# Performance work log

Hardware: AMD Instinct MI355X
Metric: run time of the kernel (lower is better)

The kernel has to match this reference:

```python
import jax, jax.numpy as jnp
import numpy as np

B, C, N = 1, 128, 8192
K, KNN, RES, NUM, NUM_LEVELS, BASE_SCALE = 128, 32, 3, 27, 3, 0.25


def _prelu(x, a):
    return jnp.where(x >= 0, x, a.reshape(()) * x)


def _gn(x, gamma, beta, groups, eps=1e-5):
    b, ch = x.shape[0], x.shape[1]
    xr = x.reshape(b, groups, -1)
    mu = xr.mean(axis=2, keepdims=True)
    var = xr.var(axis=2, keepdims=True)
    xn = ((xr - mu) * jax.lax.rsqrt(var + eps)).reshape(x.shape)
    shp = (1, ch) + (1,) * (x.ndim - 2)
    return xn * gamma.reshape(shp) + beta.reshape(shp)


def _conv1x1(x, W, b):
    y = jnp.einsum('oc,bc...->bo...', W, x)
    return y + b.reshape((1, -1) + (1,) * (x.ndim - 2))


def _base():
    i = np.arange(NUM)
    return jnp.asarray(np.stack([i // 9 % 3 - 1, i // 3 % 3 - 1, i % 3 - 1], 1).astype(np.float32))


def _forward(fmap1, fmap2, xyz2, coords,
             out_w1, out_b1, out_g, out_bt, out_pr, out_w2, out_b2,
             vox_w1, vox_b1, vox_g, vox_bt, vox_pr, vox_w2, vox_b2,
             knn_w1, knn_b1, knn_g, knn_bt, knn_pr, knn_ow, knn_ob):
    b, c, n_p = fmap1.shape
    sg = jax.lax.stop_gradient
    # correlation + truncation (init_module)
    corr = jnp.einsum('bcn,bcm->bnm', fmap1, fmap2) / jnp.sqrt(jnp.asarray(c, fmap1.dtype))
    tcorr, tidx = jax.lax.top_k(corr, K)                       # (b, n_p, K)
    bi = jnp.arange(b)[:, None, None]
    ni = jnp.arange(n_p)[None, :, None]
    txyz2 = xyz2[bi, tidx]                                     # (b, n_p, K, 3)
    ones = jnp.ones_like(tcorr)

    feats = []
    # multi-level voxel average pooling (scatter_add into 27 cubes)
    for i in range(NUM_LEVELS):
        r = BASE_SCALE * 2 ** i
        dv = jnp.round((txyz2 - coords[:, :, None, :]) / r)
        valid = jnp.all(jnp.abs(dv) <= 1.0, axis=-1)
        iv = dv + 1.0
        cube = (iv[..., 0] * 9 + iv[..., 1] * 3 + iv[..., 2]).astype(jnp.int32)
        cube = sg(jnp.where(valid, cube, 0))
        vf = sg(valid.astype(tcorr.dtype))
        cadd = jnp.zeros((b, n_p, NUM), tcorr.dtype).at[bi, ni, cube].add(tcorr * vf)
        ccnt = jnp.clip(jnp.zeros((b, n_p, NUM), tcorr.dtype).at[bi, ni, cube].add(ones * vf), 1, n_p)
        feats.append((cadd / ccnt).transpose(0, 2, 1))         # (b, 27, n_p)

    # coarse level: scatter_max to find per-cube center candidates (all no-grad)
    r = BASE_SCALE * 2 ** 3
    R = 2.0 * r
    sxyz, scrd = sg(txyz2), sg(coords)
    dv = jnp.round((sxyz - scrd[:, :, None, :]) / R)
    validc = jnp.all(jnp.abs(dv) <= 1.5, axis=-1)
    cidx = ((dv[..., 0] + 1.0) * 9 + (dv[..., 1] + 1.0) * 3 + (dv[..., 2] + 1.0)).astype(jnp.int32) + 1
    cidx = jnp.where(validc, cidx, 0)                          # (b, n_p, K) in [0, 27]
    vals = sg(tcorr) * validc
    masked = jnp.where(cidx[..., None] == jnp.arange(NUM + 1), vals[..., None], -jnp.inf)
    center_corr = masked.max(axis=2)[:, :, 1:]                 # (b, n_p, 27)
    center_idx = masked.argmax(axis=2)[:, :, 1:]
    mask_oob = center_corr <= 0                                # covers empty bins (-inf)
    center_idx = jnp.where(mask_oob, 0, center_idx)
    center_coord = sxyz[bi, ni, center_idx]                    # (b, n_p, 27, 3)

    base = _base()
    lim = (R - r) / 2.0
    idx_scatter = jnp.full((b, n_p, K), NUM, jnp.int32)
    moves = []
    for k in range(NUM):                                       # fixed 27-voxel loop
        vkc = (scrd + base[k] * R)[:, :, None, :]
        mv = jnp.clip(center_coord[:, :, k:k + 1, :] - vkc, -lim, lim) + vkc
        moves.append(mv)
        rep = jnp.all(jnp.abs((sxyz - mv) / r) <= 0.5, axis=-1) & ~mask_oob[:, :, k:k + 1]
        idx_scatter = jnp.where(rep, k, idx_scatter)           # later k overwrites (torch order)
    voxel_xyz = jnp.concatenate(moves, axis=2)                 # (b, n_p, 27, 3), no-grad

    cadd = jnp.zeros((b, n_p, NUM + 1), tcorr.dtype).at[bi, ni, idx_scatter].add(tcorr)
    ccnt = jnp.zeros((b, n_p, NUM + 1), tcorr.dtype).at[bi, ni, idx_scatter].add(ones)
    voxel_corr = cadd[:, :, :NUM] / jnp.clip(ccnt[:, :, :NUM], 1, n_p)

    vin = jnp.concatenate([voxel_corr[:, None], voxel_xyz.transpose(0, 3, 1, 2)], axis=1)  # (b,4,n_p,27)
    h = _prelu(_gn(_conv1x1(vin, vox_w1, vox_b1), vox_g, vox_bt, 8), vox_pr)
    h = _conv1x1(h, vox_w2, vox_b2)                            # (b,1,n_p,27)
    feats.append(h[:, 0].transpose(0, 2, 1))                   # (b,27,n_p)

    vfeat = jnp.concatenate(feats, axis=1)                     # (b,108,n_p)
    vfeat = _prelu(_gn(_conv1x1(vfeat, out_w1, out_b1), out_g, out_bt, 8), out_pr)
    voxel_out = _conv1x1(vfeat, out_w2, out_b2)                # (b,64,n_p)

    # knn branch
    dist = jnp.sum((txyz2 - coords[:, :, None, :]) ** 2, axis=-1)
    _, nbr = jax.lax.top_k(-sg(dist), KNN)                     # (b,n_p,KNN)
    knn_corr = jnp.take_along_axis(tcorr, nbr, axis=2)[:, None]            # (b,1,n_p,KNN)
    knn_xyz = txyz2[bi, ni, nbr].transpose(0, 3, 1, 2) - coords.transpose(0, 2, 1)[:, :, :, None]
    kf = _prelu(_gn(_conv1x1(jnp.concatenate([knn_corr, knn_xyz], 1), knn_w1, knn_b1), knn_g, knn_bt, 8), knn_pr)
    kf = kf.max(axis=3)                                        # (b,64,n_p)
    return voxel_out + _conv1x1(kf, knn_ow, knn_ob)


def setup_inputs() -> dict:
    key = jax.random.key(0)
    ks = jax.random.split(key, 26)
    xyz2 = jax.random.uniform(ks[0], (B, N, 3), jnp.float32, -3.0, 3.0)
    coords = xyz2 + 0.3 * jax.random.normal(ks[1], (B, N, 3), jnp.float32)
    w = lambda k, s, sc=0.1: sc * jax.random.normal(k, s, jnp.float32)
    return {
        'fmap1': jax.random.normal(ks[2], (B, C, N), jnp.float32),
        'fmap2': jax.random.normal(ks[3], (B, C, N), jnp.float32),
        'xyz2': xyz2, 'coords': coords,
        'out_w1': w(ks[4], (128, 108)), 'out_b1': w(ks[5], (128,)),
        'out_g': 1.0 + w(ks[6], (128,), 0.05), 'out_bt': w(ks[7], (128,), 0.05),
        'out_pr': jnp.full((1,), 0.25, jnp.float32),
        'out_w2': w(ks[8], (64, 128)), 'out_b2': w(ks[9], (64,)),
        'vox_w1': w(ks[10], (32, 4)), 'vox_b1': w(ks[11], (32,)),
        'vox_g': 1.0 + w(ks[12], (32,), 0.05), 'vox_bt': w(ks[13], (32,), 0.05),
        'vox_pr': jnp.full((1,), 0.25, jnp.float32),
        'vox_w2': w(ks[14], (1, 32)), 'vox_b2': w(ks[15], (1,)),
        'knn_w1': w(ks[16], (64, 4)), 'knn_b1': w(ks[17], (64,)),
        'knn_g': 1.0 + w(ks[18], (64,), 0.05), 'knn_bt': w(ks[19], (64,), 0.05),
        'knn_pr': jnp.full((1,), 0.25, jnp.float32),
        'knn_ow': w(ks[20], (64, 64)), 'knn_ob': w(ks[21], (64,)),
    }


def reference(fmap1, fmap2, xyz2, coords,
              out_w1, out_b1, out_g, out_bt, out_pr, out_w2, out_b2,
              vox_w1, vox_b1, vox_g, vox_bt, vox_pr, vox_w2, vox_b2,
              knn_w1, knn_b1, knn_g, knn_bt, knn_pr, knn_ow, knn_ob):
    return _forward(fmap1, fmap2, xyz2, coords,
                    out_w1, out_b1, out_g, out_bt, out_pr, out_w2, out_b2,
                    vox_w1, vox_b1, vox_g, vox_bt, vox_pr, vox_w2, vox_b2,
                    knn_w1, knn_b1, knn_g, knn_bt, knn_pr, knn_ow, knn_ob)
```

## Files before the change

kernel.cpp:

```cpp
#include <hip/hip_runtime.h>
#include <math.h>

#define NPT 8192
#define CCH 128
#define KK  128

typedef __attribute__((ext_vector_type(8))) short short8;
typedef __attribute__((ext_vector_type(4))) float f32x4;

__device__ __forceinline__ unsigned f2key(float f) {
  unsigned u = __float_as_uint(f);
  return u ^ ((u & 0x80000000u) ? 0xFFFFFFFFu : 0x80000000u);
}
__device__ __forceinline__ float key2f(unsigned k) {
  unsigned u = (k & 0x80000000u) ? (k ^ 0x80000000u) : ~k;
  return __uint_as_float(u);
}

__global__ void k_zero(double* s) {
  int t = threadIdx.x;
  if (t < 76) s[t] = 0.0;
}

__global__ __launch_bounds__(256) void k_split(const float* __restrict__ src,
                                               short* __restrict__ d0,
                                               short* __restrict__ d1,
                                               short* __restrict__ d2) {
  __shared__ float tile[2048];
  int g = blockIdx.x, t = threadIdx.x;
#pragma unroll
  for (int p = 0; p < 8; ++p) {
    int i = t + p * 256;
    int c = i >> 4, m = i & 15;
    tile[i] = src[(size_t)c * NPT + g * 16 + m];
  }
  __syncthreads();
  int o = t >> 4, m = t & 15;
  short8 w0, w1, w2;
#pragma unroll
  for (int j = 0; j < 8; ++j) {
    float a = tile[(o * 8 + j) * 16 + m];
    unsigned ua = __float_as_uint(a);
    unsigned uh = ua & 0xFFFF0000u;
    float r = a - __uint_as_float(uh);
    unsigned um = __float_as_uint(r) & 0xFFFF0000u;
    float r2 = r - __uint_as_float(um);
    unsigned ul = __float_as_uint(r2) & 0xFFFF0000u;
    w0[j] = (short)(uh >> 16);
    w1[j] = (short)(um >> 16);
    w2[j] = (short)(ul >> 16);
  }
  size_t base = (((size_t)g * 16 + o) * 16 + m) * 8;
  *(short8*)(d0 + base) = w0;
  *(short8*)(d1 + base) = w1;
  *(short8*)(d2 + base) = w2;
}

__global__ __launch_bounds__(256) void k_gemm_mfma(
    const short* __restrict__ a0, const short* __restrict__ a1, const short* __restrict__ a2,
    const short* __restrict__ b0, const short* __restrict__ b1, const short* __restrict__ b2,
    unsigned short* __restrict__ kslab, unsigned short* __restrict__ rslab, int row0) {
  __shared__ short bl[12288];
  int tid = threadIdx.x;
  int wv = tid >> 6, lane = tid & 63;
  int m15 = lane & 15, quad = lane >> 4;
  int rowgb = (row0 >> 4) + blockIdx.y * 8 + wv * 2;
  int colg0 = blockIdx.x * 8;
  f32x4 acc[2][8];
#pragma unroll
  for (int rg = 0; rg < 2; ++rg)
#pragma unroll
    for (int t = 0; t < 8; ++t) acc[rg][t] = (f32x4){0.f, 0.f, 0.f, 0.f};
#pragma unroll 1
  for (int s = 0; s < 4; ++s) {
    __syncthreads();
#pragma unroll
    for (int k = 0; k < 6; ++k) {
      int u = tid + k * 256;
      int split = u >> 9;
      int r1 = u & 511;
      int t = r1 >> 6;
      int oc = (r1 >> 4) & 3;
      int m = r1 & 15;
      const short* bp = (split == 0) ? b0 : (split == 1) ? b1 : b2;
      size_t gaddr = (((size_t)(colg0 + t) * 16 + (s * 4 + oc)) * 16 + m) * 8;
      int laddr = (((split * 8 + t) * 4 + oc) * 16 + m) * 8;
      *(short8*)(bl + laddr) = *(const short8*)(bp + gaddr);
    }
    __syncthreads();
    int oct = s * 4 + quad;
    short8 A0[2], A1[2], A2[2];
#pragma unroll
    for (int rg = 0; rg < 2; ++rg) {
      size_t ab = (((size_t)(rowgb + rg) * 16 + oct) * 16 + m15) * 8;
      A0[rg] = *(const short8*)(a0 + ab);
      A1[rg] = *(const short8*)(a1 + ab);
      A2[rg] = *(const short8*)(a2 + ab);
    }
#pragma unroll
    for (int t = 0; t < 8; ++t) {
      int lb = ((t * 4 + quad) * 16 + m15) * 8;
      short8 B0 = *(const short8*)(bl + lb);
      short8 B1 = *(const short8*)(bl + 4096 + lb);
      short8 B2 = *(const short8*)(bl + 8192 + lb);
#pragma unroll
      for (int rg = 0; rg < 2; ++rg) {
        acc[rg][t] = __builtin_amdgcn_mfma_f32_16x16x32_bf16(A2[rg], B0, acc[rg][t], 0, 0, 0);
        acc[rg][t] = __builtin_amdgcn_mfma_f32_16x16x32_bf16(A0[rg], B2, acc[rg][t], 0, 0, 0);
        acc[rg][t] = __builtin_amdgcn_mfma_f32_16x16x32_bf16(A1[rg], B1, acc[rg][t], 0, 0, 0);
        acc[rg][t] = __builtin_amdgcn_mfma_f32_16x16x32_bf16(A1[rg], B0, acc[rg][t], 0, 0, 0);
        acc[rg][t] = __builtin_amdgcn_mfma_f32_16x16x32_bf16(A0[rg], B1, acc[rg][t], 0, 0, 0);
        acc[rg][t] = __builtin_amdgcn_mfma_f32_16x16x32_bf16(A0[rg], B0, acc[rg][t], 0, 0, 0);
      }
    }
  }
#pragma unroll
  for (int rg = 0; rg < 2; ++rg) {
    int rl = (blockIdx.y * 8 + wv * 2 + rg) * 16 + quad * 4;
#pragma unroll
    for (int t = 0; t < 8; ++t) {
      int col = (colg0 + t) * 16 + m15;
#pragma unroll
      for (int r = 0; r < 4; ++r) {
        unsigned key = f2key(acc[rg][t][r]);
        kslab[(size_t)(rl + r) * NPT + col] = (unsigned short)(key >> 16);
        rslab[(size_t)(rl + r) * NPT + col] = (unsigned short)(key & 0xFFFFu);
      }
    }
  }
}

__global__ __launch_bounds__(256) void k_select16(const unsigned short* __restrict__ kslab,
                                                  const unsigned short* __restrict__ rslab,
                                                  int row0,
                                                  float* __restrict__ tcorr,
                                                  int* __restrict__ tidx) {
  __shared__ int wcnt[2][4][3];
  __shared__ int s_ntop, s_ncand;
  __shared__ unsigned candm[2048];
  const float sc = 0.08838834764831845f;
  int tid = threadIdx.x, lane = tid & 63, wv = tid >> 6;
  int rl = blockIdx.x, row = row0 + rl;
  const unsigned* rp = (const unsigned*)(kslab + (size_t)rl * NPT);
  const unsigned short* rr = rslab + (size_t)rl * NPT;
  unsigned pk[16];
#pragma unroll
  for (int j = 0; j < 16; ++j) pk[j] = rp[tid + j * 256];
  if (tid == 0) { s_ntop = 0; s_ncand = 0; }
  unsigned P = 0;
  int par = 0;
#pragma unroll 1
  for (int b = 14; b >= 0; b -= 2) {
    unsigned T1 = P | (1u << b), T2 = P | (2u << b), T3 = P | (3u << b);
    int c1 = 0, c2 = 0, c3 = 0;
#pragma unroll
    for (int j = 0; j < 16; ++j) {
      unsigned klo = pk[j] & 0xFFFFu, khi = pk[j] >> 16;
      c1 += (klo >= T1) ? 1 : 0; c1 += (khi >= T1) ? 1 : 0;
      c2 += (klo >= T2) ? 1 : 0; c2 += (khi >= T2) ? 1 : 0;
      c3 += (klo >= T3) ? 1 : 0; c3 += (khi >= T3) ? 1 : 0;
    }
    for (int off = 32; off; off >>= 1) {
      c1 += __shfl_down(c1, off); c2 += __shfl_down(c2, off); c3 += __shfl_down(c3, off);
    }
    __syncthreads();
    if (lane == 0) { wcnt[par][wv][0] = c1; wcnt[par][wv][1] = c2; wcnt[par][wv][2] = c3; }
    __syncthreads();
    int t1 = wcnt[par][0][0] + wcnt[par][1][0] + wcnt[par][2][0] + wcnt[par][3][0];
    int t2 = wcnt[par][0][1] + wcnt[par][1][1] + wcnt[par][2][1] + wcnt[par][3][1];
    int t3 = wcnt[par][0][2] + wcnt[par][1][2] + wcnt[par][2][2] + wcnt[par][3][2];
    if (t3 >= KK) P = T3;
    else if (t2 >= KK) P = T2;
    else if (t1 >= KK) P = T1;
    par ^= 1;
  }
  int base = row * KK;
#pragma unroll
  for (int j = 0; j < 16; ++j) {
    unsigned klo = pk[j] & 0xFFFFu, khi = pk[j] >> 16;
    int col0 = (tid + j * 256) * 2;
    if (klo > P) {
      int p = atomicAdd(&s_ntop, 1);
      unsigned k32 = (klo << 16) | (unsigned)rr[col0];
      tcorr[base + p] = key2f(k32) * sc;
      tidx[base + p] = col0;
    } else if (klo == P) {
      int c = atomicAdd(&s_ncand, 1);
      if (c < 2048) candm[c] = (((unsigned)rr[col0]) << 13) | (unsigned)(8191 - col0);
    }
    if (khi > P) {
      int p = atomicAdd(&s_ntop, 1);
      unsigned k32 = (khi << 16) | (unsigned)rr[col0 + 1];
      tcorr[base + p] = key2f(k32) * sc;
      tidx[base + p] = col0 + 1;
    } else if (khi == P) {
      int c = atomicAdd(&s_ncand, 1);
      if (c < 2048) candm[c] = (((unsigned)rr[col0 + 1]) << 13) | (unsigned)(8191 - col0 - 1);
    }
  }
  __syncthreads();
  int ntop = s_ntop;
  int nc = s_ncand < 2048 ? s_ncand : 2048;
  int krem = KK - ntop;
  for (int ci = tid; ci < nc; ci += 256) {
    unsigned mi = candm[ci];
    int r = 0;
    for (int j = 0; j < nc; ++j) r += (candm[j] > mi) ? 1 : 0;
    if (r < krem) {
      unsigned res = mi >> 13;
      int col = 8191 - (int)(mi & 0x1FFFu);
      unsigned k32 = (P << 16) | res;
      tcorr[base + ntop + r] = key2f(k32) * sc;
      tidx[base + ntop + r] = col;
    }
  }
}

__global__ __launch_bounds__(128) void k_point(const float* __restrict__ tcorr,
                                               const int* __restrict__ tidx,
                                               const float* __restrict__ xyz2,
                                               const float* __restrict__ coords,
                                               float* __restrict__ feats,
                                               float* __restrict__ vox_in,
                                               float* __restrict__ knn_in) {
  __shared__ float px[128], py[128], pz[128];
  __shared__ float4 dd4s[32];
  __shared__ float cadd[81], ccnt[81];
  __shared__ unsigned long long cmax[27];
  __shared__ unsigned long long gmax;
  __shared__ float4 mvp[27];
  __shared__ float vadd[28];
  __shared__ int vcnt[28];
  int n = blockIdx.x, t = threadIdx.x;
  float v = tcorr[(size_t)n * KK + t];
  int idx = tidx[(size_t)n * KK + t];
  float p0 = xyz2[idx * 3 + 0], p1 = xyz2[idx * 3 + 1], p2 = xyz2[idx * 3 + 2];
  float c0 = coords[n * 3 + 0], c1 = coords[n * 3 + 1], c2 = coords[n * 3 + 2];
  px[t] = p0; py[t] = p1; pz[t] = p2;
  float dx = p0 - c0, dy = p1 - c1, dz = p2 - c2;
  float d = dx * dx + dy * dy + dz * dz;
  ((float*)dd4s)[t] = d;
  if (t < 81) { cadd[t] = 0.f; ccnt[t] = 0.f; }
  if (t < 27) cmax[t] = 0ULL;
  if (t < 28) { vadd[t] = 0.f; vcnt[t] = 0; }
  if (t == 0) gmax = 0ULL;
  __syncthreads();
#pragma unroll
  for (int lvl = 0; lvl < 3; ++lvl) {
    float rinv = (lvl == 0) ? 4.f : (lvl == 1) ? 2.f : 1.f;
    float d0 = rintf(dx * rinv), d1 = rintf(dy * rinv), d2 = rintf(dz * rinv);
    if (fabsf(d0) <= 1.f && fabsf(d1) <= 1.f && fabsf(d2) <= 1.f) {
      int cube = (int)(d0 + 1.f) * 9 + (int)(d1 + 1.f) * 3 + (int)(d2 + 1.f);
      atomicAdd(&cadd[lvl * 27 + cube], v);
      atomicAdd(&ccnt[lvl * 27 + cube], 1.f);
    }
  }
  unsigned long long pk = (((unsigned long long)f2key(v)) << 32) | (unsigned)t;
  atomicMax(&gmax, pk);
  {
    float d0 = rintf(dx * 0.25f), d1 = rintf(dy * 0.25f), d2 = rintf(dz * 0.25f);
    if (fabsf(d0) <= 1.5f && fabsf(d1) <= 1.5f && fabsf(d2) <= 1.5f) {
      int bin = (int)(d0 + 1.f) * 9 + (int)(d1 + 1.f) * 3 + (int)(d2 + 1.f);
      atomicMax(&cmax[bin], pk);
    }
  }
  __syncthreads();
  if (t < 27) {
    unsigned long long pkb = cmax[t];
    unsigned hi = (unsigned)(pkb >> 32);
    int ob = (hi <= 0x80000000u) ? 1 : 0;
    int ki = ob ? (int)(gmax & 0xFFFFFFFFULL) : (int)(pkb & 0xFFFFFFFFULL);
    float ccx = px[ki], ccy = py[ki], ccz = pz[ki];
    float bx = (float)(t / 9 - 1), by = (float)((t / 3) % 3 - 1), bz = (float)(t % 3 - 1);
    float vk0 = c0 + bx * 4.f, vk1 = c1 + by * 4.f, vk2 = c2 + bz * 4.f;
    float m0 = fminf(fmaxf(ccx - vk0, -1.f), 1.f) + vk0;
    float m1 = fminf(fmaxf(ccy - vk1, -1.f), 1.f) + vk1;
    float m2 = fminf(fmaxf(ccz - vk2, -1.f), 1.f) + vk2;
    mvp[t] = make_float4(m0, m1, m2, ob ? 1.f : 0.f);
    float* vp = vox_in + ((size_t)n * 27 + t) * 4;
    vp[1] = m0; vp[2] = m1; vp[3] = m2;
  }
  __syncthreads();
  int is = 27;
#pragma unroll 1
  for (int b = 0; b < 27; ++b) {
    float4 mv = mvp[b];
    if (mv.w == 0.f && fabsf(p0 - mv.x) <= 1.f && fabsf(p1 - mv.y) <= 1.f &&
        fabsf(p2 - mv.z) <= 1.f)
      is = b;
  }
  atomicAdd(&vadd[is], v);
  atomicAdd(&vcnt[is], 1);
  __syncthreads();
  if (t < 27) {
    float cnt = fmaxf((float)vcnt[t], 1.f);
    vox_in[((size_t)n * 27 + t) * 4 + 0] = vadd[t] / cnt;
  }
  if (t < 81) {
    float cnt = fminf(fmaxf(ccnt[t], 1.f), 8192.f);
    feats[(size_t)t * NPT + n] = cadd[t] / cnt;
  }
  int rank = 0;
#pragma unroll 4
  for (int j4 = 0; j4 < 32; ++j4) {
    float4 dj = dd4s[j4];
    int jb = j4 * 4;
    rank += (dj.x < d || (dj.x == d && jb + 0 < t)) ? 1 : 0;
    rank += (dj.y < d || (dj.y == d && jb + 1 < t)) ? 1 : 0;
    rank += (dj.z < d || (dj.z == d && jb + 2 < t)) ? 1 : 0;
    rank += (dj.w < d || (dj.w == d && jb + 3 < t)) ? 1 : 0;
  }
  if (rank < 32) {
    float* kp = knn_in + ((size_t)n * 32 + rank) * 4;
    *(float4*)kp = make_float4(v, dx, dy, dz);
  }
}

__global__ __launch_bounds__(256) void k_moments(const float* __restrict__ vox_in,
                                                 const float* __restrict__ knn_in,
                                                 double* __restrict__ mom) {
  int b = blockIdx.x, t = threadIdx.x;
  int isknn = (b >= 256) ? 1 : 0;
  const float* src = isknn ? knn_in : vox_in;
  int nsite = isknn ? NPT * 32 : NPT * 27;
  int base = isknn ? 14 : 0;
  int bb = isknn ? b - 256 : b;
  float S0 = 0, S1 = 0, S2 = 0, S3 = 0;
  float M00 = 0, M01 = 0, M02 = 0, M03 = 0, M11 = 0, M12 = 0, M13 = 0, M22 = 0, M23 = 0, M33 = 0;
  for (int s = bb * 256 + t; s < nsite; s += 256 * 256) {
    float4 x = *(const float4*)(src + (size_t)s * 4);
    S0 += x.x; S1 += x.y; S2 += x.z; S3 += x.w;
    M00 += x.x * x.x; M01 += x.x * x.y; M02 += x.x * x.z; M03 += x.x * x.w;
    M11 += x.y * x.y; M12 += x.y * x.z; M13 += x.y * x.w;
    M22 += x.z * x.z; M23 += x.z * x.w; M33 += x.w * x.w;
  }
  float vals[14] = {S0, S1, S2, S3, M00, M01, M02, M03, M11, M12, M13, M22, M23, M33};
  for (int off = 32; off; off >>= 1)
#pragma unroll
    for (int i = 0; i < 14; ++i) vals[i] += __shfl_down(vals[i], off);
  __shared__ float part[14];
  if (t < 14) part[t] = 0.f;
  __syncthreads();
  if ((t & 63) == 0)
#pragma unroll
    for (int i = 0; i < 14; ++i) atomicAdd(&part[i], vals[i]);
  __syncthreads();
  if (t < 14) atomicAdd(&mom[base + t], (double)part[t]);
}

__global__ void k_stats_fin(const float* __restrict__ vw1, const float* __restrict__ vb1,
                            const float* __restrict__ kw1, const float* __restrict__ kb1,
                            const double* __restrict__ mom, double* __restrict__ stats) {
  int t = threadIdx.x;
  if (t >= 16) return;
  int isknn = (t >= 8) ? 1 : 0;
  const double* m = mom + (isknn ? 14 : 0);
  const float* W = isknn ? kw1 : vw1;
  const float* Bi = isknn ? kb1 : vb1;
  double N = isknn ? (double)NPT * 32.0 : (double)NPT * 27.0;
  int per = isknn ? 8 : 4;
  int g = isknn ? t - 8 : t;
  double S0 = m[0], S1 = m[1], S2 = m[2], S3 = m[3];
  double M00 = m[4], M01 = m[5], M02 = m[6], M03 = m[7];
  double M11 = m[8], M12 = m[9], M13 = m[10], M22 = m[11], M23 = m[12], M33 = m[13];
  double sum = 0.0, ssq = 0.0;
  for (int k = 0; k < per; ++k) {
    int oc = g * per + k;
    double w0 = W[oc * 4 + 0], w1 = W[oc * 4 + 1], w2 = W[oc * 4 + 2], w3 = W[oc * 4 + 3];
    double b = Bi[oc];
    double ws = w0 * S0 + w1 * S1 + w2 * S2 + w3 * S3;
    double q = w0 * w0 * M00 + w1 * w1 * M11 + w2 * w2 * M22 + w3 * w3 * M33 +
               2.0 * (w0 * w1 * M01 + w0 * w2 * M02 + w0 * w3 * M03 +
                      w1 * w2 * M12 + w1 * w3 * M13 + w2 * w3 * M23);
    sum += ws + N * b;
    ssq += q + 2.0 * b * ws + N * b * b;
  }
  double* out = stats + (isknn ? 16 : 0);
  out[2 * g + 0] = sum;
  out[2 * g + 1] = ssq;
}

__global__ __launch_bounds__(256) void k_vox_apply(const float* __restrict__ vox_in,
                                                   const float* __restrict__ w1,
                                                   const float* __restrict__ b1,
                                                   const float* __restrict__ gamma,
                                                   const float* __restrict__ beta,
                                                   const float* __restrict__ pr,
                                                   const float* __restrict__ w2,
                                                   const float* __restrict__ b2,
                                                   const double* __restrict__ stats,
                                                   float* __restrict__ feats) {
  int s = blockIdx.x * 256 + threadIdx.x;
  if (s >= NPT * 27) return;
  float mean[8], rstd[8];
  const double cntd = 4.0 * 8192.0 * 27.0;
#pragma unroll
  for (int g = 0; g < 8; ++g) {
    double m = stats[2 * g] / cntd;
    double var = stats[2 * g + 1] / cntd - m * m;
    mean[g] = (float)m;
    rstd[g] = (float)(1.0 / sqrt(var + 1e-5));
  }
  float a = pr[0];
  float4 in = *(const float4*)(vox_in + (size_t)s * 4);
  float out = b2[0];
#pragma unroll
  for (int oc = 0; oc < 32; ++oc) {
    float4 w = *(const float4*)(w1 + oc * 4);
    float h = w.x * in.x + w.y * in.y + w.z * in.z + w.w * in.w + b1[oc];
    int g = oc >> 2;
    float xn = (h - mean[g]) * rstd[g] * gamma[oc] + beta[oc];
    float y = (xn >= 0.f) ? xn : a * xn;
    out += w2[oc] * y;
  }
  int n = s / 27, bb = s - n * 27;
  feats[(size_t)(81 + bb) * NPT + n] = out;
}

__global__ __launch_bounds__(256) void k_knn_max(const float* __restrict__ knn_in,
                                                 const float* __restrict__ w1,
                                                 const float* __restrict__ b1,
                                                 const float* __restrict__ gamma,
                                                 const float* __restrict__ beta,
                                                 const float* __restrict__ pr,
                                                 const double* __restrict__ stats,
                                                 float* __restrict__ kf) {
  int tid0 = blockIdx.x * 256 + threadIdx.x;
  int n = tid0 & (NPT - 1);
  int oc = tid0 >> 13;
  const double cntd = 8.0 * 8192.0 * 32.0;
  int g = oc >> 3;
  double md = stats[2 * g] / cntd;
  double var = stats[2 * g + 1] / cntd - md * md;
  float mean = (float)md, rstd = (float)(1.0 / sqrt(var + 1e-5));
  float4 w = *(const float4*)(w1 + oc * 4);
  float bb = b1[oc], ga = gamma[oc], be = beta[oc], a = pr[0];
  float mx = -INFINITY;
  for (int j = 0; j < 32; ++j) {
    float4 in = *(const float4*)(knn_in + ((size_t)n * 32 + j) * 4);
    float h = w.x * in.x + w.y * in.y + w.z * in.z + w.w * in.w + bb;
    float xn = (h - mean) * rstd * ga + be;
    float y = (xn >= 0.f) ? xn : a * xn;
    mx = fmaxf(mx, y);
  }
  kf[(size_t)oc * NPT + n] = mx;
}

__global__ __launch_bounds__(256) void k_out1(const float* __restrict__ feats,
                                              const float* __restrict__ w1,
                                              const float* __restrict__ b1,
                                              float* __restrict__ h1,
                                              double* __restrict__ stats) {
  __shared__ float wlds[108 * 16];
  __shared__ float ls, lq;
  int t = threadIdx.x;
  int ocb = blockIdx.y * 16;
  for (int i = t; i < 108 * 16; i += 256) {
    int j = i / 108, ic = i - j * 108;
    wlds[ic * 16 + j] = w1[ocb * 108 + i];
  }
  if (t == 0) { ls = 0.f; lq = 0.f; }
  __syncthreads();
  int n = blockIdx.x * 256 + t;
  float acc[16];
#pragma unroll
  for (int j = 0; j < 16; ++j) acc[j] = b1[ocb + j];
#pragma unroll 4
  for (int ic = 0; ic < 108; ++ic) {
    float v = feats[(size_t)ic * NPT + n];
    const float4* w4 = (const float4*)(wlds + ic * 16);
#pragma unroll
    for (int q = 0; q < 4; ++q) {
      float4 w = w4[q];
      acc[q * 4 + 0] += w.x * v; acc[q * 4 + 1] += w.y * v;
      acc[q * 4 + 2] += w.z * v; acc[q * 4 + 3] += w.w * v;
    }
  }
  float s = 0.f, q = 0.f;
#pragma unroll
  for (int j = 0; j < 16; ++j) {
    h1[(size_t)(ocb + j) * NPT + n] = acc[j];
    s += acc[j]; q += acc[j] * acc[j];
  }
  for (int off = 32; off; off >>= 1) { s += __shfl_down(s, off); q += __shfl_down(q, off); }
  if ((t & 63) == 0) { atomicAdd(&ls, s); atomicAdd(&lq, q); }
  __syncthreads();
  if (t == 0) {
    atomicAdd(&stats[2 * blockIdx.y + 0], (double)ls);
    atomicAdd(&stats[2 * blockIdx.y + 1], (double)lq);
  }
}

__global__ __launch_bounds__(256) void k_final(const float* __restrict__ h1,
                                               const float* __restrict__ kf,
                                               const float* __restrict__ gamma,
                                               const float* __restrict__ beta,
                                               const float* __restrict__ pr,
                                               const float* __restrict__ w2,
                                               const float* __restrict__ b2,
                                               const float* __restrict__ kow,
                                               const float* __restrict__ kob,
                                               const double* __restrict__ stats,
                                               float* __restrict__ out) {
  __shared__ float wl[192 * 8];
  __shared__ float scl[128], sft[128];
  int t = threadIdx.x;
  int ocb = blockIdx.y * 8;
  for (int i = t; i < 128 * 8; i += 256) {
    int j = i >> 7, ic = i & 127;
    wl[ic * 8 + j] = w2[(ocb + j) * 128 + ic];
  }
  for (int i = t; i < 64 * 8; i += 256) {
    int j = i >> 6, ic = i & 63;
    wl[(128 + ic) * 8 + j] = kow[(ocb + j) * 64 + ic];
  }
  if (t < 128) {
    const double cntd = 16.0 * 8192.0;
    int g = t >> 4;
    double m = stats[2 * g] / cntd;
    double var = stats[2 * g + 1] / cntd - m * m;
    float rs = (float)(1.0 / sqrt(var + 1e-5));
    float ga = gamma[t];
    scl[t] = rs * ga;
    sft[t] = beta[t] - (float)m * rs * ga;
  }
  __syncthreads();
  int n = blockIdx.x * 256 + t;
  float a = pr[0];
  float acc[8];
#pragma unroll
  for (int j = 0; j < 8; ++j) acc[j] = b2[ocb + j] + kob[ocb + j];
#pragma unroll 2
  for (int ic = 0; ic < 128; ++ic) {
    float x = h1[(size_t)ic * NPT + n];
    float xn = x * scl[ic] + sft[ic];
    float y = (xn >= 0.f) ? xn : a * xn;
    const float4* w4 = (const float4*)(wl + ic * 8);
    float4 wa = w4[0], wb = w4[1];
    acc[0] += wa.x * y; acc[1] += wa.y * y; acc[2] += wa.z * y; acc[3] += wa.w * y;
    acc[4] += wb.x * y; acc[5] += wb.y * y; acc[6] += wb.z * y; acc[7] += wb.w * y;
  }
#pragma unroll 2
  for (int ic = 0; ic < 64; ++ic) {
    float y = kf[(size_t)ic * NPT + n];
    const float4* w4 = (const float4*)(wl + (128 + ic) * 8);
    float4 wa = w4[0], wb = w4[1];
    acc[0] += wa.x * y; acc[1] += wa.y * y; acc[2] += wa.z * y; acc[3] += wa.w * y;
    acc[4] += wb.x * y; acc[5] += wb.y * y; acc[6] += wb.z * y; acc[7] += wb.w * y;
  }
#pragma unroll
  for (int j = 0; j < 8; ++j)
    out[(size_t)(ocb + j) * NPT + n] = acc[j];
}

extern "C" void kernel_launch(void* const* d_in, const int* in_sizes, int n_in,
                              void* d_out, int out_size, void* d_ws, size_t ws_size,
                              hipStream_t stream) {
  (void)in_sizes; (void)n_in; (void)out_size;
  const float* fmap1  = (const float*)d_in[0];
  const float* fmap2  = (const float*)d_in[1];
  const float* xyz2   = (const float*)d_in[2];
  const float* coords = (const float*)d_in[3];
  const float* out_w1 = (const float*)d_in[4];
  const float* out_b1 = (const float*)d_in[5];
  const float* out_g  = (const float*)d_in[6];
  const float* out_bt = (const float*)d_in[7];
  const float* out_pr = (const float*)d_in[8];
  const float* out_w2 = (const float*)d_in[9];
  const float* out_b2 = (const float*)d_in[10];
  const float* vox_w1 = (const float*)d_in[11];
  const float* vox_b1 = (const float*)d_in[12];
  const float* vox_g  = (const float*)d_in[13];
  const float* vox_bt = (const float*)d_in[14];
  const float* vox_pr = (const float*)d_in[15];
  const float* vox_w2 = (const float*)d_in[16];
  const float* vox_b2 = (const float*)d_in[17];
  const float* knn_w1 = (const float*)d_in[18];
  const float* knn_b1 = (const float*)d_in[19];
  const float* knn_g  = (const float*)d_in[20];
  const float* knn_bt = (const float*)d_in[21];
  const float* knn_pr = (const float*)d_in[22];
  const float* knn_ow = (const float*)d_in[23];
  const float* knn_ob = (const float*)d_in[24];

  float* ws = (float*)d_ws;
  const size_t nonslab = 9633944ull;
  int SR;
  if (ws_size >= (33554432ull + nonslab) * 4ull + 4096ull) SR = 4096;
  else if (ws_size >= (16777216ull + nonslab) * 4ull + 4096ull) SR = 2048;
  else if (ws_size >= (8388608ull + nonslab) * 4ull + 4096ull) SR = 1024;
  else SR = 512;

  unsigned short* kslab = (unsigned short*)ws;
  unsigned short* rslab = kslab + (size_t)SR * NPT;
  float* after  = ws + (size_t)SR * NPT;
  float* tcorr  = after;
  int*   tidx   = (int*)(tcorr + (size_t)NPT * KK);
  float* feats  = tcorr + (size_t)NPT * KK * 2;
  float* vox_in = feats + 108 * NPT;
  float* knn_in = vox_in + (size_t)NPT * 27 * 4;
  float* h1     = knn_in + (size_t)NPT * 32 * 4;
  float* kf     = h1 + 128 * NPT;
  double* stats = (double*)(kf + 64 * NPT);
  double* mom   = stats + 48;
  short* a0s    = (short*)(mom + 28);
  short* a1s    = a0s + (size_t)NPT * CCH;
  short* a2s    = a1s + (size_t)NPT * CCH;
  short* b0s    = a2s + (size_t)NPT * CCH;
  short* b1s    = b0s + (size_t)NPT * CCH;
  short* b2s    = b1s + (size_t)NPT * CCH;

  hipLaunchKernelGGL(k_zero, dim3(1), dim3(128), 0, stream, stats);
  hipLaunchKernelGGL(k_split, dim3(NPT / 16), dim3(256), 0, stream, fmap1, a0s, a1s, a2s);
  hipLaunchKernelGGL(k_split, dim3(NPT / 16), dim3(256), 0, stream, fmap2, b0s, b1s, b2s);
  int iters = NPT / SR;
  for (int s = 0; s < iters; ++s) {
    hipLaunchKernelGGL(k_gemm_mfma, dim3(NPT / 128, SR / 128), dim3(256), 0, stream,
                       a0s, a1s, a2s, b0s, b1s, b2s, kslab, rslab, s * SR);
    hipLaunchKernelGGL(k_select16, dim3(SR), dim3(256), 0, stream, kslab, rslab, s * SR,
                       tcorr, tidx);
  }
  hipLaunchKernelGGL(k_point, dim3(NPT), dim3(128), 0, stream, tcorr, tidx, xyz2, coords,
                     feats, vox_in, knn_in);
  hipLaunchKernelGGL(k_moments, dim3(512), dim3(256), 0, stream, vox_in, knn_in, mom);
  hipLaunchKernelGGL(k_stats_fin, dim3(1), dim3(64), 0, stream, vox_w1, vox_b1, knn_w1, knn_b1,
                     mom, stats);
  hipLaunchKernelGGL(k_vox_apply, dim3((NPT * 27 + 255) / 256), dim3(256), 0, stream, vox_in,
                     vox_w1, vox_b1, vox_g, vox_bt, vox_pr, vox_w2, vox_b2, stats, feats);
  hipLaunchKernelGGL(k_knn_max, dim3(64 * NPT / 256), dim3(256), 0, stream, knn_in, knn_w1,
                     knn_b1, knn_g, knn_bt, knn_pr, stats + 16, kf);
  hipLaunchKernelGGL(k_out1, dim3(NPT / 256, 8), dim3(256), 0, stream, feats, out_w1, out_b1, h1,
                     stats + 32);
  hipLaunchKernelGGL(k_final, dim3(NPT / 256, 8), dim3(256), 0, stream, h1, kf, out_g, out_bt,
                     out_pr, out_w2, out_b2, knn_ow, knn_ob, stats + 32, (float*)d_out);
}
```

Before: 517.7 us.

## Store full 32-bit sort keys in one slab and count radix bins with ballot

The GEMM now writes the full 32-bit order-preserving key per correlation entry into a single slab instead of splitting it into separate high and low 16-bit slabs. The select kernel loads 32 keys per thread, compares against thresholds shifted into the upper half, and counts hits with wave ballot plus popcount instead of per-lane counters and shuffle reductions. This removes the scattered second reads of the low-half slab during output and candidate collection, and it replaces the per-lane packing work. In exchange it keeps twice as many registers live per thread and issues one ballot per element per threshold.

```diff
diff --git a/kernel.cpp b/kernel.cpp
--- a/kernel.cpp
+++ b/kernel.cpp
@@ -59,7 +59,7 @@
 __global__ __launch_bounds__(256) void k_gemm_mfma(
     const short* __restrict__ a0, const short* __restrict__ a1, const short* __restrict__ a2,
     const short* __restrict__ b0, const short* __restrict__ b1, const short* __restrict__ b2,
-    unsigned short* __restrict__ kslab, unsigned short* __restrict__ rslab, int row0) {
+    unsigned* __restrict__ kslab, int row0) {
   __shared__ short bl[12288];
   int tid = threadIdx.x;
   int wv = tid >> 6, lane = tid & 63;
@@ -121,17 +121,13 @@
     for (int t = 0; t < 8; ++t) {
       int col = (colg0 + t) * 16 + m15;
 #pragma unroll
-      for (int r = 0; r < 4; ++r) {
-        unsigned key = f2key(acc[rg][t][r]);
-        kslab[(size_t)(rl + r) * NPT + col] = (unsigned short)(key >> 16);
-        rslab[(size_t)(rl + r) * NPT + col] = (unsigned short)(key & 0xFFFFu);
-      }
-    }
-  }
-}
-
-__global__ __launch_bounds__(256) void k_select16(const unsigned short* __restrict__ kslab,
-                                                  const unsigned short* __restrict__ rslab,
+      for (int r = 0; r < 4; ++r)
+        kslab[(size_t)(rl + r) * NPT + col] = f2key(acc[rg][t][r]);
+    }
+  }
+}
+
+__global__ __launch_bounds__(256) void k_select32(const unsigned* __restrict__ kslab,
                                                   int row0,
                                                   float* __restrict__ tcorr,
                                                   int* __restrict__ tidx) {
@@ -141,27 +137,23 @@
   const float sc = 0.08838834764831845f;
   int tid = threadIdx.x, lane = tid & 63, wv = tid >> 6;
   int rl = blockIdx.x, row = row0 + rl;
-  const unsigned* rp = (const unsigned*)(kslab + (size_t)rl * NPT);
-  const unsigned short* rr = rslab + (size_t)rl * NPT;
-  unsigned pk[16];
-#pragma unroll
-  for (int j = 0; j < 16; ++j) pk[j] = rp[tid + j * 256];
+  const unsigned* rp = kslab + (size_t)rl * NPT;
+  unsigned pk[32];
+#pragma unroll
+  for (int j = 0; j < 32; ++j) pk[j] = rp[tid + j * 256];
   if (tid == 0) { s_ntop = 0; s_ncand = 0; }
   unsigned P = 0;
   int par = 0;
 #pragma unroll 1
   for (int b = 14; b >= 0; b -= 2) {
-    unsigned T1 = P | (1u << b), T2 = P | (2u << b), T3 = P | (3u << b);
+    unsigned T1 = (P | (1u << b)) << 16, T2 = (P | (2u << b)) << 16, T3 = (P | (3u << b)) << 16;
     int c1 = 0, c2 = 0, c3 = 0;
 #pragma unroll
-    for (int j = 0; j < 16; ++j) {
-      unsigned klo = pk[j] & 0xFFFFu, khi = pk[j] >> 16;
-      c1 += (klo >= T1) ? 1 : 0; c1 += (khi >= T1) ? 1 : 0;
-      c2 += (klo >= T2) ? 1 : 0; c2 += (khi >= T2) ? 1 : 0;
-      c3 += (klo >= T3) ? 1 : 0; c3 += (khi >= T3) ? 1 : 0;
-    }
-    for (int off = 32; off; off >>= 1) {
-      c1 += __shfl_down(c1, off); c2 += __shfl_down(c2, off); c3 += __shfl_down(c3, off);
+    for (int j = 0; j < 32; ++j) {
+      unsigned k = pk[j];
+      c1 += (int)__popcll(__ballot(k >= T1));
+      c2 += (int)__popcll(__ballot(k >= T2));
+      c3 += (int)__popcll(__ballot(k >= T3));
     }
     __syncthreads();
     if (lane == 0) { wcnt[par][wv][0] = c1; wcnt[par][wv][1] = c2; wcnt[par][wv][2] = c3; }
@@ -169,33 +161,24 @@
     int t1 = wcnt[par][0][0] + wcnt[par][1][0] + wcnt[par][2][0] + wcnt[par][3][0];
     int t2 = wcnt[par][0][1] + wcnt[par][1][1] + wcnt[par][2][1] + wcnt[par][3][1];
     int t3 = wcnt[par][0][2] + wcnt[par][1][2] + wcnt[par][2][2] + wcnt[par][3][2];
-    if (t3 >= KK) P = T3;
-    else if (t2 >= KK) P = T2;
-    else if (t1 >= KK) P = T1;
+    if (t3 >= KK) P |= (3u << b);
+    else if (t2 >= KK) P |= (2u << b);
+    else if (t1 >= KK) P |= (1u << b);
     par ^= 1;
   }
   int base = row * KK;
 #pragma unroll
-  for (int j = 0; j < 16; ++j) {
-    unsigned klo = pk[j] & 0xFFFFu, khi = pk[j] >> 16;
-    int col0 = (tid + j * 256) * 2;
-    if (klo > P) {
+  for (int j = 0; j < 32; ++j) {
+    unsigned k = pk[j];
+    unsigned kh = k >> 16;
+    int col = tid + j * 256;
+    if (kh > P) {
       int p = atomicAdd(&s_ntop, 1);
-      unsigned k32 = (klo << 16) | (unsigned)rr[col0];
-      tcorr[base + p] = key2f(k32) * sc;
-      tidx[base + p] = col0;
-    } else if (klo == P) {
+      tcorr[base + p] = key2f(k) * sc;
+      tidx[base + p] = col;
+    } else if (kh == P) {
       int c = atomicAdd(&s_ncand, 1);
-      if (c < 2048) candm[c] = (((unsigned)rr[col0]) << 13) | (unsigned)(8191 - col0);
-    }
-    if (khi > P) {
-      int p = atomicAdd(&s_ntop, 1);
-      unsigned k32 = (khi << 16) | (unsigned)rr[col0 + 1];
-      tcorr[base + p] = key2f(k32) * sc;
-      tidx[base + p] = col0 + 1;
-    } else if (khi == P) {
-      int c = atomicAdd(&s_ncand, 1);
-      if (c < 2048) candm[c] = (((unsigned)rr[col0 + 1]) << 13) | (unsigned)(8191 - col0 - 1);
+      if (c < 2048) candm[c] = ((k & 0xFFFFu) << 13) | (unsigned)(8191 - col);
     }
   }
   __syncthreads();
@@ -591,8 +574,7 @@
   else if (ws_size >= (8388608ull + nonslab) * 4ull + 4096ull) SR = 1024;
   else SR = 512;
 
-  unsigned short* kslab = (unsigned short*)ws;
-  unsigned short* rslab = kslab + (size_t)SR * NPT;
+  unsigned* kslab = (unsigned*)ws;
   float* after  = ws + (size_t)SR * NPT;
   float* tcorr  = after;
   int*   tidx   = (int*)(tcorr + (size_t)NPT * KK);
@@ -616,8 +598,8 @@
   int iters = NPT / SR;
   for (int s = 0; s < iters; ++s) {
     hipLaunchKernelGGL(k_gemm_mfma, dim3(NPT / 128, SR / 128), dim3(256), 0, stream,
-                       a0s, a1s, a2s, b0s, b1s, b2s, kslab, rslab, s * SR);
-    hipLaunchKernelGGL(k_select16, dim3(SR), dim3(256), 0, stream, kslab, rslab, s * SR,
+                       a0s, a1s, a2s, b0s, b1s, b2s, kslab, s * SR);
+    hipLaunchKernelGGL(k_select32, dim3(SR), dim3(256), 0, stream, kslab, s * SR,
                        tcorr, tidx);
   }
   hipLaunchKernelGGL(k_point, dim3(NPT), dim3(128), 0, stream, tcorr, tidx, xyz2, coords,
```

Measured after the change: 569.8 us. +10.1%, slower.

## Use 1-bit radix passes in top-k select, fold stats finalize into consumers

Applied to the files above, without the earlier changes.

The per-row top-k radix select now unpacks the 16-bit keys into 32 registers. It refines the threshold one bit per pass, with one counter and a single barrier per pass, instead of three counters and two barriers per 2-bit pass. The separate single-block stats finalize kernel is removed. Its double-precision group mean and rstd math is recomputed inside k_vox_apply and k_knn_max from the raw moments, which saves a launch but adds redundant per-thread FP64 work. A larger slab size (SR=8192) is also allowed when the workspace is big enough, cutting the number of gemm/select launch pairs.

```diff
diff --git a/kernel.cpp b/kernel.cpp
--- a/kernel.cpp
+++ b/kernel.cpp
@@ -135,7 +135,7 @@
                                                   int row0,
                                                   float* __restrict__ tcorr,
                                                   int* __restrict__ tidx) {
-  __shared__ int wcnt[2][4][3];
+  __shared__ int wcnt[2][4];
   __shared__ int s_ntop, s_ncand;
   __shared__ unsigned candm[2048];
   const float sc = 0.08838834764831845f;
@@ -143,59 +143,42 @@
   int rl = blockIdx.x, row = row0 + rl;
   const unsigned* rp = (const unsigned*)(kslab + (size_t)rl * NPT);
   const unsigned short* rr = rslab + (size_t)rl * NPT;
-  unsigned pk[16];
-#pragma unroll
-  for (int j = 0; j < 16; ++j) pk[j] = rp[tid + j * 256];
+  unsigned k16[32];
+#pragma unroll
+  for (int j = 0; j < 16; ++j) {
+    unsigned p = rp[tid + j * 256];
+    k16[2 * j] = p & 0xFFFFu;
+    k16[2 * j + 1] = p >> 16;
+  }
   if (tid == 0) { s_ntop = 0; s_ncand = 0; }
   unsigned P = 0;
   int par = 0;
 #pragma unroll 1
-  for (int b = 14; b >= 0; b -= 2) {
-    unsigned T1 = P | (1u << b), T2 = P | (2u << b), T3 = P | (3u << b);
-    int c1 = 0, c2 = 0, c3 = 0;
-#pragma unroll
-    for (int j = 0; j < 16; ++j) {
-      unsigned klo = pk[j] & 0xFFFFu, khi = pk[j] >> 16;
-      c1 += (klo >= T1) ? 1 : 0; c1 += (khi >= T1) ? 1 : 0;
-      c2 += (klo >= T2) ? 1 : 0; c2 += (khi >= T2) ? 1 : 0;
-      c3 += (klo >= T3) ? 1 : 0; c3 += (khi >= T3) ? 1 : 0;
-    }
-    for (int off = 32; off; off >>= 1) {
-      c1 += __shfl_down(c1, off); c2 += __shfl_down(c2, off); c3 += __shfl_down(c3, off);
-    }
+  for (int b = 15; b >= 0; --b) {
+    unsigned T = P | (1u << b);
+    int c = 0;
+#pragma unroll
+    for (int j = 0; j < 32; ++j) c += (k16[j] >= T) ? 1 : 0;
+    for (int off = 32; off; off >>= 1) c += __shfl_down(c, off);
+    if (lane == 0) wcnt[par][wv] = c;
     __syncthreads();
-    if (lane == 0) { wcnt[par][wv][0] = c1; wcnt[par][wv][1] = c2; wcnt[par][wv][2] = c3; }
-    __syncthreads();
-    int t1 = wcnt[par][0][0] + wcnt[par][1][0] + wcnt[par][2][0] + wcnt[par][3][0];
-    int t2 = wcnt[par][0][1] + wcnt[par][1][1] + wcnt[par][2][1] + wcnt[par][3][1];
-    int t3 = wcnt[par][0][2] + wcnt[par][1][2] + wcnt[par][2][2] + wcnt[par][3][2];
-    if (t3 >= KK) P = T3;
-    else if (t2 >= KK) P = T2;
-    else if (t1 >= KK) P = T1;
+    int tot = wcnt[par][0] + wcnt[par][1] + wcnt[par][2] + wcnt[par][3];
+    if (tot >= KK) P = T;
     par ^= 1;
   }
   int base = row * KK;
 #pragma unroll
-  for (int j = 0; j < 16; ++j) {
-    unsigned klo = pk[j] & 0xFFFFu, khi = pk[j] >> 16;
-    int col0 = (tid + j * 256) * 2;
-    if (klo > P) {
+  for (int j = 0; j < 32; ++j) {
+    unsigned kh = k16[j];
+    int col = (tid + (j >> 1) * 256) * 2 + (j & 1);
+    if (kh > P) {
       int p = atomicAdd(&s_ntop, 1);
-      unsigned k32 = (klo << 16) | (unsigned)rr[col0];
+      unsigned k32 = (kh << 16) | (unsigned)rr[col];
       tcorr[base + p] = key2f(k32) * sc;
-      tidx[base + p] = col0;
-    } else if (klo == P) {
+      tidx[base + p] = col;
+    } else if (kh == P) {
       int c = atomicAdd(&s_ncand, 1);
-      if (c < 2048) candm[c] = (((unsigned)rr[col0]) << 13) | (unsigned)(8191 - col0);
-    }
-    if (khi > P) {
-      int p = atomicAdd(&s_ntop, 1);
-      unsigned k32 = (khi << 16) | (unsigned)rr[col0 + 1];
-      tcorr[base + p] = key2f(k32) * sc;
-      tidx[base + p] = col0 + 1;
-    } else if (khi == P) {
-      int c = atomicAdd(&s_ncand, 1);
-      if (c < 2048) candm[c] = (((unsigned)rr[col0 + 1]) << 13) | (unsigned)(8191 - col0 - 1);
+      if (c < 2048) candm[c] = (((unsigned)rr[col]) << 13) | (unsigned)(8191 - col);
     }
   }
   __syncthreads();
@@ -348,18 +331,9 @@
   if (t < 14) atomicAdd(&mom[base + t], (double)part[t]);
 }
 
-__global__ void k_stats_fin(const float* __restrict__ vw1, const float* __restrict__ vb1,
-                            const float* __restrict__ kw1, const float* __restrict__ kb1,
-                            const double* __restrict__ mom, double* __restrict__ stats) {
-  int t = threadIdx.x;
-  if (t >= 16) return;
-  int isknn = (t >= 8) ? 1 : 0;
-  const double* m = mom + (isknn ? 14 : 0);
-  const float* W = isknn ? kw1 : vw1;
-  const float* Bi = isknn ? kb1 : vb1;
-  double N = isknn ? (double)NPT * 32.0 : (double)NPT * 27.0;
-  int per = isknn ? 8 : 4;
-  int g = isknn ? t - 8 : t;
+__device__ __forceinline__ void group_stats(const double* m, const float* W, const float* Bi,
+                                            double N, int per, int g,
+                                            float* mean_out, float* rstd_out) {
   double S0 = m[0], S1 = m[1], S2 = m[2], S3 = m[3];
   double M00 = m[4], M01 = m[5], M02 = m[6], M03 = m[7];
   double M11 = m[8], M12 = m[9], M13 = m[10], M22 = m[11], M23 = m[12], M33 = m[13];
@@ -375,9 +349,11 @@
     sum += ws + N * b;
     ssq += q + 2.0 * b * ws + N * b * b;
   }
-  double* out = stats + (isknn ? 16 : 0);
-  out[2 * g + 0] = sum;
-  out[2 * g + 1] = ssq;
+  double cnt = N * (double)per;
+  double mm = sum / cnt;
+  double var = ssq / cnt - mm * mm;
+  *mean_out = (float)mm;
+  *rstd_out = (float)(1.0 / sqrt(var + 1e-5));
 }
 
 __global__ __launch_bounds__(256) void k_vox_apply(const float* __restrict__ vox_in,
@@ -388,19 +364,14 @@
                                                    const float* __restrict__ pr,
                                                    const float* __restrict__ w2,
                                                    const float* __restrict__ b2,
-                                                   const double* __restrict__ stats,
+                                                   const double* __restrict__ mom,
                                                    float* __restrict__ feats) {
   int s = blockIdx.x * 256 + threadIdx.x;
   if (s >= NPT * 27) return;
   float mean[8], rstd[8];
-  const double cntd = 4.0 * 8192.0 * 27.0;
-#pragma unroll
-  for (int g = 0; g < 8; ++g) {
-    double m = stats[2 * g] / cntd;
-    double var = stats[2 * g + 1] / cntd - m * m;
-    mean[g] = (float)m;
-    rstd[g] = (float)(1.0 / sqrt(var + 1e-5));
-  }
+#pragma unroll
+  for (int g = 0; g < 8; ++g)
+    group_stats(mom, w1, b1, (double)NPT * 27.0, 4, g, &mean[g], &rstd[g]);
   float a = pr[0];
   float4 in = *(const float4*)(vox_in + (size_t)s * 4);
   float out = b2[0];
@@ -423,16 +394,13 @@
                                                  const float* __restrict__ gamma,
                                                  const float* __restrict__ beta,
                                                  const float* __restrict__ pr,
-                                                 const double* __restrict__ stats,
+                                                 const double* __restrict__ mom,
                                                  float* __restrict__ kf) {
   int tid0 = blockIdx.x * 256 + threadIdx.x;
   int n = tid0 & (NPT - 1);
   int oc = tid0 >> 13;
-  const double cntd = 8.0 * 8192.0 * 32.0;
-  int g = oc >> 3;
-  double md = stats[2 * g] / cntd;
-  double var = stats[2 * g + 1] / cntd - md * md;
-  float mean = (float)md, rstd = (float)(1.0 / sqrt(var + 1e-5));
+  float mean, rstd;
+  group_stats(mom, w1, b1, (double)NPT * 32.0, 8, oc >> 3, &mean, &rstd);
   float4 w = *(const float4*)(w1 + oc * 4);
   float bb = b1[oc], ga = gamma[oc], be = beta[oc], a = pr[0];
   float mx = -INFINITY;
@@ -586,7 +554,8 @@
   float* ws = (float*)d_ws;
   const size_t nonslab = 9633944ull;
   int SR;
-  if (ws_size >= (33554432ull + nonslab) * 4ull + 4096ull) SR = 4096;
+  if (ws_size >= (67108864ull + nonslab) * 4ull + 4096ull) SR = 8192;
+  else if (ws_size >= (33554432ull + nonslab) * 4ull + 4096ull) SR = 4096;
   else if (ws_size >= (16777216ull + nonslab) * 4ull + 4096ull) SR = 2048;
   else if (ws_size >= (8388608ull + nonslab) * 4ull + 4096ull) SR = 1024;
   else SR = 512;
@@ -623,12 +592,10 @@
   hipLaunchKernelGGL(k_point, dim3(NPT), dim3(128), 0, stream, tcorr, tidx, xyz2, coords,
                      feats, vox_in, knn_in);
   hipLaunchKernelGGL(k_moments, dim3(512), dim3(256), 0, stream, vox_in, knn_in, mom);
-  hipLaunchKernelGGL(k_stats_fin, dim3(1), dim3(64), 0, stream, vox_w1, vox_b1, knn_w1, knn_b1,
-                     mom, stats);
   hipLaunchKernelGGL(k_vox_apply, dim3((NPT * 27 + 255) / 256), dim3(256), 0, stream, vox_in,
-                     vox_w1, vox_b1, vox_g, vox_bt, vox_pr, vox_w2, vox_b2, stats, feats);
+                     vox_w1, vox_b1, vox_g, vox_bt, vox_pr, vox_w2, vox_b2, mom, feats);
   hipLaunchKernelGGL(k_knn_max, dim3(64 * NPT / 256), dim3(256), 0, stream, knn_in, knn_w1,
-                     knn_b1, knn_g, knn_bt, knn_pr, stats + 16, kf);
+                     knn_b1, knn_g, knn_bt, knn_pr, mom + 14, kf);
   hipLaunchKernelGGL(k_out1, dim3(NPT / 256, 8), dim3(256), 0, stream, feats, out_w1, out_b1, h1,
                      stats + 32);
   hipLaunchKernelGGL(k_final, dim3(NPT / 256, 8), dim3(256), 0, stream, h1, kf, out_g, out_bt,
```

Result: faster. 505.9 us (-2.3%).
